# Kernel optimization log

Measured on AMD Instinct MI355X. Metric: run time of the kernel, lower is better.

The kernel has to match this reference:

```python
import jax, jax.numpy as jnp
import numpy as np

H = 128  # rnn_features


def setup_inputs() -> dict:
    key = jax.random.key(0)
    ks = jax.random.split(key, 9)
    B, T, D = 1024, 256, 128
    x = jax.random.normal(ks[0], (B, T, D), dtype=jnp.float32)
    hidden_state = jax.random.normal(ks[1], (1, B, H), dtype=jnp.float32)
    done = jax.random.randint(ks[2], (B, T), 0, 2, dtype=jnp.int32)
    s = 1.0 / np.sqrt(H)
    W_ih = jax.random.uniform(ks[3], (3 * H, D), jnp.float32, -s, s)
    W_hh = jax.random.uniform(ks[4], (3 * H, H), jnp.float32, -s, s)
    b_ih = jax.random.uniform(ks[5], (3 * H,), jnp.float32, -s, s)
    b_hh = jax.random.uniform(ks[6], (3 * H,), jnp.float32, -s, s)
    fc_W = jax.random.uniform(ks[7], (H, H), jnp.float32, -s, s)
    fc_b = jax.random.uniform(ks[8], (H,), jnp.float32, -s, s)
    return {"x": x, "hidden_state": hidden_state, "done": done,
            "W_ih": W_ih, "W_hh": W_hh, "b_ih": b_ih, "b_hh": b_hh,
            "fc_W": fc_W, "fc_b": fc_b}


def _gru_with_resets(x, h0, done, W_ih, W_hh, b_ih, b_hh):
    # x: [B,T,D], h0: [B,H], done: [B,T] int
    B, T, D = x.shape
    # reset multiplier applied BEFORE step t: 1 - done[:, t-1]; no reset at t=0
    done_f = done.astype(x.dtype)
    reset = 1.0 - jnp.concatenate([jnp.zeros((B, 1), x.dtype), done_f[:, :-1]], axis=1)  # [B,T]
    # precompute input projections in one big GEMM: [B,T,3H]
    xi = jnp.einsum('btd,gd->btg', x, W_ih) + b_ih
    xi_T = jnp.transpose(xi, (1, 0, 2))      # [T,B,3H]
    reset_T = jnp.transpose(reset, (1, 0))   # [T,B]

    def step(h, inp):
        xi_t, r_t = inp
        h = h * r_t[:, None]
        gh = h @ W_hh.T + b_hh               # [B,3H]
        r = jax.nn.sigmoid(xi_t[:, :H] + gh[:, :H])
        z = jax.nn.sigmoid(xi_t[:, H:2 * H] + gh[:, H:2 * H])
        n = jnp.tanh(xi_t[:, 2 * H:] + r * gh[:, 2 * H:])
        h = (1.0 - z) * n + z * h
        return h, h

    h_last, hs = jax.lax.scan(step, h0, (xi_T, reset_T))
    return jnp.transpose(hs, (1, 0, 2)), h_last  # [B,T,H], [B,H]


def reference(x, hidden_state, done, W_ih, W_hh, b_ih, b_hh, fc_W, fc_b):
    # body_net is identity; fcs = Linear + ELU
    rfeat, h_last = _gru_with_resets(x, hidden_state[0], done, W_ih, W_hh, b_ih, b_hh)
    out = jax.nn.elu(jnp.einsum('bth,oh->bto', rfeat, fc_W) + fc_b)
    return out, h_last[None]  # hidden back to [1,B,H]
```

## Files before the change

kernel.cpp:

```cpp
#include <hip/hip_runtime.h>
#include <hip/hip_bf16.h>
#include <math.h>

#define Hd 128
#define Tt 256
#define Bb 1024
#define CL 16
#define NCK (Tt / CL)

typedef __attribute__((ext_vector_type(8))) short short8;
typedef __attribute__((ext_vector_type(4))) float f32x4;

__device__ __forceinline__ short f2bf(float f) {
    unsigned u = __float_as_uint(f);
    u += 0x7fffu + ((u >> 16) & 1u);
    return (short)(u >> 16);
}
__device__ __forceinline__ float bflo(unsigned u) { return __uint_as_float(u << 16); }
__device__ __forceinline__ float bfhi(unsigned u) { return __uint_as_float(u & 0xffff0000u); }

__global__ void prep_weights(const float* __restrict__ Wih,
                             const float* __restrict__ Whh,
                             const float* __restrict__ fcW,
                             short* __restrict__ oIh, short* __restrict__ oHh,
                             short* __restrict__ oFc) {
    int t = blockIdx.x * 256 + threadIdx.x;
    if (t >= 14336) return;
    const float* src;
    short* dst;
    if (t < 6144)       { src = Wih; dst = oIh + t * 8; }
    else if (t < 12288) { t -= 6144;  src = Whh; dst = oHh + t * 8; }
    else                { t -= 12288; src = fcW; dst = oFc + t * 8; }
    int lane = t & 63, kf = (t >> 6) & 3, nt = t >> 8;
    const float* s = src + (nt * 16 + (lane & 15)) * 128 + kf * 32 + 8 * (lane >> 4);
#pragma unroll
    for (int j = 0; j < 8; j++) dst[j] = f2bf(s[j]);
}

__global__ __launch_bounds__(512)
void xi_gemm(const float* __restrict__ x, const float* __restrict__ bih,
             const float* __restrict__ bhh, const short* __restrict__ wIh,
             short* __restrict__ xi_l) {
    __shared__ short xs[64 * 136];
    const int tid = threadIdx.x, wv = tid >> 6, ln = tid & 63;
    const int q = ln & 15, lg = ln >> 4;
    const int bg = blockIdx.x;
    const int sl0 = blockIdx.y * 4;
    {
        const int row = tid >> 3, kq = tid & 7;
        const int b = row & 15, dt = row >> 4;
        const float* xp = x + (((size_t)(bg * 16 + b)) * Tt + (sl0 + dt)) * Hd + kq * 16;
        f32x4 u0 = *(const f32x4*)&xp[0],  u1 = *(const f32x4*)&xp[4];
        f32x4 u2 = *(const f32x4*)&xp[8],  u3 = *(const f32x4*)&xp[12];
        short8 s0, s1;
#pragma unroll
        for (int i = 0; i < 4; i++) { s0[i] = f2bf(u0[i]); s0[i+4] = f2bf(u1[i]);
                                      s1[i] = f2bf(u2[i]); s1[i+4] = f2bf(u3[i]); }
        *(short8*)&xs[row * 136 + kq * 16] = s0;
        *(short8*)&xs[row * 136 + kq * 16 + 8] = s1;
    }
    __syncthreads();
    short8 wb[3][4];
#pragma unroll
    for (int i = 0; i < 3; i++)
#pragma unroll
        for (int kf = 0; kf < 4; kf++)
            wb[i][kf] = *(const short8*)&wIh[(((wv + 8 * i) * 4 + kf) * 64 + ln) * 8];
    float biasv[3];
#pragma unroll
    for (int i = 0; i < 3; i++) {
        int c = (wv + 8 * i) * 16 + q;
        biasv[i] = bih[c] + (c < 256 ? bhh[c] : 0.f);
    }
#pragma unroll 1
    for (int mt = 0; mt < 4; mt++) {
        short8 af[4];
#pragma unroll
        for (int kf = 0; kf < 4; kf++)
            af[kf] = *(const short8*)&xs[(mt * 16 + q) * 136 + kf * 32 + 8 * lg];
        f32x4 c0 = {0,0,0,0}, c1 = {0,0,0,0}, c2 = {0,0,0,0};
#pragma unroll
        for (int kf = 0; kf < 4; kf++) {
            c0 = __builtin_amdgcn_mfma_f32_16x16x32_bf16(af[kf], wb[0][kf], c0, 0, 0, 0);
            c1 = __builtin_amdgcn_mfma_f32_16x16x32_bf16(af[kf], wb[1][kf], c1, 0, 0, 0);
            c2 = __builtin_amdgcn_mfma_f32_16x16x32_bf16(af[kf], wb[2][kf], c2, 0, 0, 0);
        }
#pragma unroll
        for (int i = 0; i < 3; i++) {
            f32x4 cc = (i == 0) ? c0 : (i == 1) ? c1 : c2;
            unsigned d0 = (unsigned)(unsigned short)f2bf(cc[0] + biasv[i]) |
                          ((unsigned)(unsigned short)f2bf(cc[1] + biasv[i]) << 16);
            unsigned d1 = (unsigned)(unsigned short)f2bf(cc[2] + biasv[i]) |
                          ((unsigned)(unsigned short)f2bf(cc[3] + biasv[i]) << 16);
            uint2 dd = {d0, d1};
            ((uint2*)xi_l)[(((size_t)bg * Tt + (sl0 + mt)) * 24 + (wv + 8 * i)) * 64 + ln] = dd;
        }
    }
}

__global__ __launch_bounds__(256)
void gru_chunk(const short* __restrict__ xi_l, const int* __restrict__ done,
               const float* __restrict__ h0,
               const float* __restrict__ bhh, const float* __restrict__ fcb,
               const short* __restrict__ wHh, const short* __restrict__ wFc,
               float* __restrict__ out, float* __restrict__ hlast) {
    __shared__ short hT[2][16 * 136];
    __shared__ int doneL[Tt * 16];
    __shared__ int rbL[16];
    const int tid = threadIdx.x, j = tid >> 6, ln = tid & 63;
    const int q = ln & 15, lg = ln >> 4;
    const int bg = blockIdx.x, ck = blockIdx.y;
    const int t_c = ck * CL, t_end = t_c + CL;

    {
        const int b = tid >> 4, i = tid & 15;
        const int* dp = done + (size_t)(bg * 16 + b) * Tt;
        for (int t = i; t < t_end; t += 16) doneL[t * 16 + b] = dp[t];
    }
    __syncthreads();
    if (tid < 16) {
        int r = 0;
        for (int t = t_c - 1; t >= 0; --t)
            if (doneL[t * 16 + tid]) { r = t + 1; break; }
        rbL[tid] = r;
    }
    __syncthreads();
    int rmin = rbL[0];
#pragma unroll
    for (int b = 1; b < 16; b++) rmin = min(rmin, rbL[b]);

    short8 whh[6][4], wfc[2][4];
#pragma unroll
    for (int i = 0; i < 6; i++)
#pragma unroll
        for (int kf = 0; kf < 4; kf++)
            whh[i][kf] = *(const short8*)&wHh[(((j + 4 * i) * 4 + kf) * 64 + ln) * 8];
#pragma unroll
    for (int cs = 0; cs < 2; cs++)
#pragma unroll
        for (int kf = 0; kf < 4; kf++)
            wfc[cs][kf] = *(const short8*)&wFc[(((j + 4 * cs) * 4 + kf) * 64 + ln) * 8];
    float cbn[2], cbf[2];
#pragma unroll
    for (int cs = 0; cs < 2; cs++) {
        int c = 16 * j + 64 * cs + q;
        cbn[cs] = bhh[256 + c];
        cbf[cs] = fcb[c];
    }

    float h_reg[2][4];
#pragma unroll
    for (int cs = 0; cs < 2; cs++)
#pragma unroll
        for (int r = 0; r < 4; r++) {
            int bb = 4 * lg + r, c = 16 * j + 64 * cs + q;
            h_reg[cs][r] = (rbL[bb] == 0) ? h0[(size_t)(bg * 16 + bb) * Hd + c] : 0.f;
        }
    {
        int row = tid >> 4, c0 = (tid & 15) * 8;
        short8 s0 = {0,0,0,0,0,0,0,0};
        if (rbL[row] == 0) {
            const float* hp = &h0[(size_t)(bg * 16 + row) * Hd + c0];
            f32x4 u0 = *(const f32x4*)&hp[0], u1 = *(const f32x4*)&hp[4];
#pragma unroll
            for (int i = 0; i < 4; i++) { s0[i] = f2bf(u0[i]); s0[i+4] = f2bf(u1[i]); }
        }
        *(short8*)&hT[rmin & 1][row * 136 + c0] = s0;
    }
    __syncthreads();

    const uint2* xp = (const uint2*)xi_l + ((size_t)bg * Tt + rmin) * 1536 + j * 64 + ln;
    uint2 cur[6];
#pragma unroll
    for (int i = 0; i < 6; i++) cur[i] = xp[i * 256];
    xp += 1536;

#pragma unroll 1
    for (int t = rmin; t < t_end; ++t) {
        const short* hTp = &hT[t & 1][0];
        short* hTn = &hT[(t + 1) & 1][0];
        short8 haf[4];
#pragma unroll
        for (int kf = 0; kf < 4; kf++)
            haf[kf] = *(const short8*)&hTp[q * 136 + kf * 32 + 8 * lg];

        f32x4 acc[6];
#pragma unroll
        for (int i = 0; i < 4; i++) {
            f32x4 a = {bflo(cur[i].x), bfhi(cur[i].x), bflo(cur[i].y), bfhi(cur[i].y)};
            acc[i] = a;
        }
        { f32x4 a = {cbn[0], cbn[0], cbn[0], cbn[0]}; acc[4] = a; }
        { f32x4 a = {cbn[1], cbn[1], cbn[1], cbn[1]}; acc[5] = a; }
        uint2 xn8[2] = {cur[4], cur[5]};
        if (t + 1 < t_end) {
#pragma unroll
            for (int i = 0; i < 6; i++) cur[i] = xp[i * 256];
        }
        xp += 1536;

        if (t > t_c) {
            f32x4 fca[2];
            { f32x4 a = {cbf[0], cbf[0], cbf[0], cbf[0]}; fca[0] = a; }
            { f32x4 a = {cbf[1], cbf[1], cbf[1], cbf[1]}; fca[1] = a; }
#pragma unroll
            for (int kf = 0; kf < 4; kf++)
#pragma unroll
                for (int cs = 0; cs < 2; cs++)
                    fca[cs] = __builtin_amdgcn_mfma_f32_16x16x32_bf16(haf[kf], wfc[cs][kf], fca[cs], 0, 0, 0);
#pragma unroll
            for (int cs = 0; cs < 2; cs++)
#pragma unroll
                for (int r = 0; r < 4; r++) {
                    int bb = 4 * lg + r, c = 16 * j + 64 * cs + q;
                    float v = fca[cs][r];
                    float e = __expf(v) - 1.f;
                    v = v > 0.f ? v : e;
                    out[(((size_t)(bg * 16 + bb)) * Tt + (t - 1)) * Hd + c] = v;
                }
        }

        if (t > 0) {
            int dn = doneL[(t - 1) * 16 + q];
            short8 z8 = {0,0,0,0,0,0,0,0};
#pragma unroll
            for (int kf = 0; kf < 4; kf++) haf[kf] = dn ? z8 : haf[kf];
        }
#pragma unroll
        for (int kf = 0; kf < 4; kf++)
#pragma unroll
            for (int i = 0; i < 6; i++)
                acc[i] = __builtin_amdgcn_mfma_f32_16x16x32_bf16(haf[kf], whh[i][kf], acc[i], 0, 0, 0);

        float rstf[4] = {1.f, 1.f, 1.f, 1.f};
        if (t > 0) {
            int4 dd = *(const int4*)&doneL[(t - 1) * 16 + 4 * lg];
            rstf[0] = dd.x ? 0.f : 1.f; rstf[1] = dd.y ? 0.f : 1.f;
            rstf[2] = dd.z ? 0.f : 1.f; rstf[3] = dd.w ? 0.f : 1.f;
        }
#pragma unroll
        for (int cs = 0; cs < 2; cs++) {
#pragma unroll
            for (int r = 0; r < 4; r++) {
                float rg = __builtin_amdgcn_rcpf(1.f + __expf(-acc[cs][r]));
                float zg = __builtin_amdgcn_rcpf(1.f + __expf(-acc[2 + cs][r]));
                float xn = (r == 0) ? bflo(xn8[cs].x) : (r == 1) ? bfhi(xn8[cs].x)
                         : (r == 2) ? bflo(xn8[cs].y) : bfhi(xn8[cs].y);
                float aa = fmaf(rg, acc[4 + cs][r], xn);
                float ng = 1.f - 2.f * __builtin_amdgcn_rcpf(__expf(2.f * aa) + 1.f);
                float hp = h_reg[cs][r] * rstf[r];
                float hn = (1.f - zg) * ng + zg * hp;
                h_reg[cs][r] = hn;
                hTn[(4 * lg + r) * 136 + 16 * j + 64 * cs + q] = f2bf(hn);
            }
        }
        __builtin_amdgcn_sched_barrier(0);
        __builtin_amdgcn_s_waitcnt(0xC07F);
        __builtin_amdgcn_s_barrier();
        __builtin_amdgcn_sched_barrier(0);
    }
    {
        const short* hTp = &hT[t_end & 1][0];
        short8 haf[4];
#pragma unroll
        for (int kf = 0; kf < 4; kf++)
            haf[kf] = *(const short8*)&hTp[q * 136 + kf * 32 + 8 * lg];
        f32x4 fca[2];
        { f32x4 a = {cbf[0], cbf[0], cbf[0], cbf[0]}; fca[0] = a; }
        { f32x4 a = {cbf[1], cbf[1], cbf[1], cbf[1]}; fca[1] = a; }
#pragma unroll
        for (int kf = 0; kf < 4; kf++)
#pragma unroll
            for (int cs = 0; cs < 2; cs++)
                fca[cs] = __builtin_amdgcn_mfma_f32_16x16x32_bf16(haf[kf], wfc[cs][kf], fca[cs], 0, 0, 0);
#pragma unroll
        for (int cs = 0; cs < 2; cs++)
#pragma unroll
            for (int r = 0; r < 4; r++) {
                int bb = 4 * lg + r, c = 16 * j + 64 * cs + q;
                float v = fca[cs][r];
                float e = __expf(v) - 1.f;
                v = v > 0.f ? v : e;
                out[(((size_t)(bg * 16 + bb)) * Tt + (t_end - 1)) * Hd + c] = v;
            }
    }
    if (ck == NCK - 1) {
#pragma unroll
        for (int cs = 0; cs < 2; cs++)
#pragma unroll
            for (int r = 0; r < 4; r++) {
                int bb = 4 * lg + r, c = 16 * j + 64 * cs + q;
                hlast[(size_t)(bg * 16 + bb) * Hd + c] = h_reg[cs][r];
            }
    }
}

extern "C" void kernel_launch(void* const* d_in, const int* in_sizes, int n_in,
                              void* d_out, int out_size, void* d_ws, size_t ws_size,
                              hipStream_t stream) {
    const float* x   = (const float*)d_in[0];
    const float* h0  = (const float*)d_in[1];
    const int*   dn  = (const int*)d_in[2];
    const float* Wih = (const float*)d_in[3];
    const float* Whh = (const float*)d_in[4];
    const float* bih = (const float*)d_in[5];
    const float* bhh = (const float*)d_in[6];
    const float* fcW = (const float*)d_in[7];
    const float* fcb = (const float*)d_in[8];

    short* wIh = (short*)d_ws;
    short* wHh = wIh + 49152;
    short* wFc = wHh + 49152;
    short* xi_l = wFc + 16384;
    float* out = (float*)d_out;
    float* hlast = out + (size_t)Bb * Tt * Hd;

    prep_weights<<<56, 256, 0, stream>>>(Wih, Whh, fcW, wIh, wHh, wFc);
    xi_gemm<<<dim3(64, Tt / 4), 512, 0, stream>>>(x, bih, bhh, wIh, xi_l);
    gru_chunk<<<dim3(64, NCK), 256, 0, stream>>>(xi_l, dn, h0, bhh, fcb,
                                                 wHh, wFc, out, hlast);
}
```

Before: 177.4 us.

## Split GRU chunk work across eight waves instead of four per block

The recurrent GRU kernel now runs 512 threads per block, and each wave owns a single 16-column slice of the hidden state instead of two. Per wave, the MFMA count, the weight registers and the gate math per step are halved, which shortens the serial critical path of each timestep. The cost is more waves synchronising at the per-step barrier and twice the threads contending for the same shared hidden-state buffer. Each thread also holds fewer registers.

```diff
diff --git a/kernel.cpp b/kernel.cpp
--- a/kernel.cpp
+++ b/kernel.cpp
@@ -98,7 +98,7 @@
     }
 }
 
-__global__ __launch_bounds__(256)
+__global__ __launch_bounds__(512)
 void gru_chunk(const short* __restrict__ xi_l, const int* __restrict__ done,
                const float* __restrict__ h0,
                const float* __restrict__ bhh, const float* __restrict__ fcb,
@@ -107,15 +107,16 @@
     __shared__ short hT[2][16 * 136];
     __shared__ int doneL[Tt * 16];
     __shared__ int rbL[16];
-    const int tid = threadIdx.x, j = tid >> 6, ln = tid & 63;
+    const int tid = threadIdx.x, w = tid >> 6, ln = tid & 63;
     const int q = ln & 15, lg = ln >> 4;
     const int bg = blockIdx.x, ck = blockIdx.y;
     const int t_c = ck * CL, t_end = t_c + CL;
+    const int c = 16 * w + q;
 
     {
-        const int b = tid >> 4, i = tid & 15;
+        const int b = tid >> 5, i = tid & 31;
         const int* dp = done + (size_t)(bg * 16 + b) * Tt;
-        for (int t = i; t < t_end; t += 16) doneL[t * 16 + b] = dp[t];
+        for (int t = i; t < t_end; t += 32) doneL[t * 16 + b] = dp[t];
     }
     __syncthreads();
     if (tid < 16) {
@@ -129,34 +130,25 @@
 #pragma unroll
     for (int b = 1; b < 16; b++) rmin = min(rmin, rbL[b]);
 
-    short8 whh[6][4], wfc[2][4];
-#pragma unroll
-    for (int i = 0; i < 6; i++)
-#pragma unroll
-        for (int kf = 0; kf < 4; kf++)
-            whh[i][kf] = *(const short8*)&wHh[(((j + 4 * i) * 4 + kf) * 64 + ln) * 8];
-#pragma unroll
-    for (int cs = 0; cs < 2; cs++)
-#pragma unroll
-        for (int kf = 0; kf < 4; kf++)
-            wfc[cs][kf] = *(const short8*)&wFc[(((j + 4 * cs) * 4 + kf) * 64 + ln) * 8];
-    float cbn[2], cbf[2];
-#pragma unroll
-    for (int cs = 0; cs < 2; cs++) {
-        int c = 16 * j + 64 * cs + q;
-        cbn[cs] = bhh[256 + c];
-        cbf[cs] = fcb[c];
-    }
-
-    float h_reg[2][4];
-#pragma unroll
-    for (int cs = 0; cs < 2; cs++)
-#pragma unroll
-        for (int r = 0; r < 4; r++) {
-            int bb = 4 * lg + r, c = 16 * j + 64 * cs + q;
-            h_reg[cs][r] = (rbL[bb] == 0) ? h0[(size_t)(bg * 16 + bb) * Hd + c] : 0.f;
-        }
-    {
+    short8 whh[3][4], wfc[4];
+#pragma unroll
+    for (int i = 0; i < 3; i++)
+#pragma unroll
+        for (int kf = 0; kf < 4; kf++)
+            whh[i][kf] = *(const short8*)&wHh[(((w + 8 * i) * 4 + kf) * 64 + ln) * 8];
+#pragma unroll
+    for (int kf = 0; kf < 4; kf++)
+        wfc[kf] = *(const short8*)&wFc[((w * 4 + kf) * 64 + ln) * 8];
+    const float cbn = bhh[256 + c];
+    const float cbf = fcb[c];
+
+    float h_reg[4];
+#pragma unroll
+    for (int r = 0; r < 4; r++) {
+        int bb = 4 * lg + r;
+        h_reg[r] = (rbL[bb] == 0) ? h0[(size_t)(bg * 16 + bb) * Hd + c] : 0.f;
+    }
+    if (tid < 256) {
         int row = tid >> 4, c0 = (tid & 15) * 8;
         short8 s0 = {0,0,0,0,0,0,0,0};
         if (rbL[row] == 0) {
@@ -169,10 +161,10 @@
     }
     __syncthreads();
 
-    const uint2* xp = (const uint2*)xi_l + ((size_t)bg * Tt + rmin) * 1536 + j * 64 + ln;
-    uint2 cur[6];
-#pragma unroll
-    for (int i = 0; i < 6; i++) cur[i] = xp[i * 256];
+    const uint2* xp = (const uint2*)xi_l + ((size_t)bg * Tt + rmin) * 1536 + w * 64 + ln;
+    uint2 cur[3];
+#pragma unroll
+    for (int i = 0; i < 3; i++) cur[i] = xp[i * 512];
     xp += 1536;
 
 #pragma unroll 1
@@ -184,40 +176,30 @@
         for (int kf = 0; kf < 4; kf++)
             haf[kf] = *(const short8*)&hTp[q * 136 + kf * 32 + 8 * lg];
 
-        f32x4 acc[6];
-#pragma unroll
-        for (int i = 0; i < 4; i++) {
-            f32x4 a = {bflo(cur[i].x), bfhi(cur[i].x), bflo(cur[i].y), bfhi(cur[i].y)};
-            acc[i] = a;
-        }
-        { f32x4 a = {cbn[0], cbn[0], cbn[0], cbn[0]}; acc[4] = a; }
-        { f32x4 a = {cbn[1], cbn[1], cbn[1], cbn[1]}; acc[5] = a; }
-        uint2 xn8[2] = {cur[4], cur[5]};
+        f32x4 acc[3];
+        { f32x4 a = {bflo(cur[0].x), bfhi(cur[0].x), bflo(cur[0].y), bfhi(cur[0].y)}; acc[0] = a; }
+        { f32x4 a = {bflo(cur[1].x), bfhi(cur[1].x), bflo(cur[1].y), bfhi(cur[1].y)}; acc[1] = a; }
+        { f32x4 a = {cbn, cbn, cbn, cbn}; acc[2] = a; }
+        uint2 xn8 = cur[2];
         if (t + 1 < t_end) {
 #pragma unroll
-            for (int i = 0; i < 6; i++) cur[i] = xp[i * 256];
+            for (int i = 0; i < 3; i++) cur[i] = xp[i * 512];
         }
         xp += 1536;
 
         if (t > t_c) {
-            f32x4 fca[2];
-            { f32x4 a = {cbf[0], cbf[0], cbf[0], cbf[0]}; fca[0] = a; }
-            { f32x4 a = {cbf[1], cbf[1], cbf[1], cbf[1]}; fca[1] = a; }
+            f32x4 fca = {cbf, cbf, cbf, cbf};
 #pragma unroll
             for (int kf = 0; kf < 4; kf++)
-#pragma unroll
-                for (int cs = 0; cs < 2; cs++)
-                    fca[cs] = __builtin_amdgcn_mfma_f32_16x16x32_bf16(haf[kf], wfc[cs][kf], fca[cs], 0, 0, 0);
-#pragma unroll
-            for (int cs = 0; cs < 2; cs++)
-#pragma unroll
-                for (int r = 0; r < 4; r++) {
-                    int bb = 4 * lg + r, c = 16 * j + 64 * cs + q;
-                    float v = fca[cs][r];
-                    float e = __expf(v) - 1.f;
-                    v = v > 0.f ? v : e;
-                    out[(((size_t)(bg * 16 + bb)) * Tt + (t - 1)) * Hd + c] = v;
-                }
+                fca = __builtin_amdgcn_mfma_f32_16x16x32_bf16(haf[kf], wfc[kf], fca, 0, 0, 0);
+#pragma unroll
+            for (int r = 0; r < 4; r++) {
+                int bb = 4 * lg + r;
+                float v = fca[r];
+                float e = __expf(v) - 1.f;
+                v = v > 0.f ? v : e;
+                out[(((size_t)(bg * 16 + bb)) * Tt + (t - 1)) * Hd + c] = v;
+            }
         }
 
         if (t > 0) {
@@ -227,10 +209,11 @@
             for (int kf = 0; kf < 4; kf++) haf[kf] = dn ? z8 : haf[kf];
         }
 #pragma unroll
-        for (int kf = 0; kf < 4; kf++)
-#pragma unroll
-            for (int i = 0; i < 6; i++)
-                acc[i] = __builtin_amdgcn_mfma_f32_16x16x32_bf16(haf[kf], whh[i][kf], acc[i], 0, 0, 0);
+        for (int kf = 0; kf < 4; kf++) {
+            acc[0] = __builtin_amdgcn_mfma_f32_16x16x32_bf16(haf[kf], whh[0][kf], acc[0], 0, 0, 0);
+            acc[1] = __builtin_amdgcn_mfma_f32_16x16x32_bf16(haf[kf], whh[1][kf], acc[1], 0, 0, 0);
+            acc[2] = __builtin_amdgcn_mfma_f32_16x16x32_bf16(haf[kf], whh[2][kf], acc[2], 0, 0, 0);
+        }
 
         float rstf[4] = {1.f, 1.f, 1.f, 1.f};
         if (t > 0) {
@@ -239,20 +222,17 @@
             rstf[2] = dd.z ? 0.f : 1.f; rstf[3] = dd.w ? 0.f : 1.f;
         }
 #pragma unroll
-        for (int cs = 0; cs < 2; cs++) {
-#pragma unroll
-            for (int r = 0; r < 4; r++) {
-                float rg = __builtin_amdgcn_rcpf(1.f + __expf(-acc[cs][r]));
-                float zg = __builtin_amdgcn_rcpf(1.f + __expf(-acc[2 + cs][r]));
-                float xn = (r == 0) ? bflo(xn8[cs].x) : (r == 1) ? bfhi(xn8[cs].x)
-                         : (r == 2) ? bflo(xn8[cs].y) : bfhi(xn8[cs].y);
-                float aa = fmaf(rg, acc[4 + cs][r], xn);
-                float ng = 1.f - 2.f * __builtin_amdgcn_rcpf(__expf(2.f * aa) + 1.f);
-                float hp = h_reg[cs][r] * rstf[r];
-                float hn = (1.f - zg) * ng + zg * hp;
-                h_reg[cs][r] = hn;
-                hTn[(4 * lg + r) * 136 + 16 * j + 64 * cs + q] = f2bf(hn);
-            }
+        for (int r = 0; r < 4; r++) {
+            float rg = __builtin_amdgcn_rcpf(1.f + __expf(-acc[0][r]));
+            float zg = __builtin_amdgcn_rcpf(1.f + __expf(-acc[1][r]));
+            float xn = (r == 0) ? bflo(xn8.x) : (r == 1) ? bfhi(xn8.x)
+                     : (r == 2) ? bflo(xn8.y) : bfhi(xn8.y);
+            float aa = fmaf(rg, acc[2][r], xn);
+            float ng = 1.f - 2.f * __builtin_amdgcn_rcpf(__expf(2.f * aa) + 1.f);
+            float hp = h_reg[r] * rstf[r];
+            float hn = (1.f - zg) * ng + zg * hp;
+            h_reg[r] = hn;
+            hTn[(4 * lg + r) * 136 + c] = f2bf(hn);
         }
         __builtin_amdgcn_sched_barrier(0);
         __builtin_amdgcn_s_waitcnt(0xC07F);
@@ -265,33 +245,25 @@
 #pragma unroll
         for (int kf = 0; kf < 4; kf++)
             haf[kf] = *(const short8*)&hTp[q * 136 + kf * 32 + 8 * lg];
-        f32x4 fca[2];
-        { f32x4 a = {cbf[0], cbf[0], cbf[0], cbf[0]}; fca[0] = a; }
-        { f32x4 a = {cbf[1], cbf[1], cbf[1], cbf[1]}; fca[1] = a; }
-#pragma unroll
-        for (int kf = 0; kf < 4; kf++)
-#pragma unroll
-            for (int cs = 0; cs < 2; cs++)
-                fca[cs] = __builtin_amdgcn_mfma_f32_16x16x32_bf16(haf[kf], wfc[cs][kf], fca[cs], 0, 0, 0);
-#pragma unroll
-        for (int cs = 0; cs < 2; cs++)
-#pragma unroll
-            for (int r = 0; r < 4; r++) {
-                int bb = 4 * lg + r, c = 16 * j + 64 * cs + q;
-                float v = fca[cs][r];
-                float e = __expf(v) - 1.f;
-                v = v > 0.f ? v : e;
-                out[(((size_t)(bg * 16 + bb)) * Tt + (t_end - 1)) * Hd + c] = v;
-            }
+        f32x4 fca = {cbf, cbf, cbf, cbf};
+#pragma unroll
+        for (int kf = 0; kf < 4; kf++)
+            fca = __builtin_amdgcn_mfma_f32_16x16x32_bf16(haf[kf], wfc[kf], fca, 0, 0, 0);
+#pragma unroll
+        for (int r = 0; r < 4; r++) {
+            int bb = 4 * lg + r;
+            float v = fca[r];
+            float e = __expf(v) - 1.f;
+            v = v > 0.f ? v : e;
+            out[(((size_t)(bg * 16 + bb)) * Tt + (t_end - 1)) * Hd + c] = v;
+        }
     }
     if (ck == NCK - 1) {
 #pragma unroll
-        for (int cs = 0; cs < 2; cs++)
-#pragma unroll
-            for (int r = 0; r < 4; r++) {
-                int bb = 4 * lg + r, c = 16 * j + 64 * cs + q;
-                hlast[(size_t)(bg * 16 + bb) * Hd + c] = h_reg[cs][r];
-            }
+        for (int r = 0; r < 4; r++) {
+            int bb = 4 * lg + r;
+            hlast[(size_t)(bg * 16 + bb) * Hd + c] = h_reg[r];
+        }
     }
 }
 
@@ -317,6 +289,6 @@
 
     prep_weights<<<56, 256, 0, stream>>>(Wih, Whh, fcW, wIh, wHh, wFc);
     xi_gemm<<<dim3(64, Tt / 4), 512, 0, stream>>>(x, bih, bhh, wIh, xi_l);
-    gru_chunk<<<dim3(64, NCK), 256, 0, stream>>>(xi_l, dn, h0, bhh, fcb,
+    gru_chunk<<<dim3(64, NCK), 512, 0, stream>>>(xi_l, dn, h0, bhh, fcb,
                                                  wHh, wFc, out, hlast);
 }
```

Measured after the change: 198.0 us. +11.6%, slower.
